# Performance work log

Measured on AMD Instinct MI355X. Metric: run time of the kernel, lower is better.

The kernel has to match this reference:

```python
import jax, jax.numpy as jnp
import numpy as np

NEG_SLOPE = 0.2
NEG_INF = -1e9


def _gat_branch(x, src, dst, edge_type, t, W, a_src, a_dst, b):
    """Single-head PyG GATConv restricted (by masking) to edges with edge_type == t,
    with self-loops added (PyG default add_self_loops=True)."""
    N = x.shape[0]
    h = x @ W                                   # [N, out_dim]
    s = h @ a_src                               # [N] source attention term
    d = h @ a_dst                               # [N] destination attention term
    # real edges (masked by type)
    e_edge = jax.nn.leaky_relu(s[src] + d[dst], NEG_SLOPE)
    e_edge = jnp.where(edge_type == t, e_edge, NEG_INF)
    # self-loop edges i -> i
    e_self = jax.nn.leaky_relu(s + d, NEG_SLOPE)
    dst_all = jnp.concatenate([dst, jnp.arange(N)])          # [E+N]
    e_all = jnp.concatenate([e_edge, e_self])                 # [E+N]
    # softmax over incoming edges per destination node (segment softmax)
    m = jax.ops.segment_max(e_all, dst_all, num_segments=N)
    p = jnp.exp(e_all - m[dst_all])
    denom = jax.ops.segment_sum(p, dst_all, num_segments=N)
    alpha = p / denom[dst_all]                                 # [E+N]
    msg = jnp.concatenate([h[src], h], axis=0) * alpha[:, None]
    return jax.ops.segment_sum(msg, dst_all, num_segments=N) + b


def setup_inputs() -> dict:
    key = jax.random.key(0)
    ks = jax.random.split(key, 12)
    N, E, in_dim, out_dim = 100000, 1000000, 64, 64
    glorot = (6.0 / (in_dim + out_dim)) ** 0.5
    att = (6.0 / (1 + out_dim)) ** 0.5
    return {
        "x": jax.random.normal(ks[0], (N, in_dim), dtype=jnp.float32),
        "edge_index": jax.random.randint(ks[1], (2, E), 0, N),
        "edge_type": jax.random.randint(ks[2], (E,), 0, 2),
        "W_login": jax.random.uniform(ks[3], (in_dim, out_dim), jnp.float32, -glorot, glorot),
        "a_src_login": jax.random.uniform(ks[4], (out_dim,), jnp.float32, -att, att),
        "a_dst_login": jax.random.uniform(ks[5], (out_dim,), jnp.float32, -att, att),
        "b_login": jnp.zeros((out_dim,), jnp.float32),
        "W_exec": jax.random.uniform(ks[6], (in_dim, out_dim), jnp.float32, -glorot, glorot),
        "a_src_exec": jax.random.uniform(ks[7], (out_dim,), jnp.float32, -att, att),
        "a_dst_exec": jax.random.uniform(ks[8], (out_dim,), jnp.float32, -att, att),
        "b_exec": jnp.zeros((out_dim,), jnp.float32),
    }


def reference(x, edge_index, edge_type, W_login, a_src_login, a_dst_login, b_login,
              W_exec, a_src_exec, a_dst_exec, b_exec):
    src, dst = edge_index[0], edge_index[1]
    out = _gat_branch(x, src, dst, edge_type, 0, W_login, a_src_login, a_dst_login, b_login)
    out = out + _gat_branch(x, src, dst, edge_type, 1, W_exec, a_src_exec, a_dst_exec, b_exec)
    return out
```

## Files before the change

### kernel.cpp

```cpp
#include <hip/hip_runtime.h>

#define D 64
#define CAP 896
#define BINB 64

typedef unsigned short u16;
typedef __attribute__((ext_vector_type(8))) __bf16 bf16x8;
typedef __attribute__((ext_vector_type(4))) float f32x4;

__device__ __forceinline__ float lrelu(float x) { return x > 0.f ? x : 0.2f * x; }
__device__ __forceinline__ u16 f2bf(float f) {
    unsigned u = __float_as_uint(f);
    return (u16)((u + 0x7fffu + ((u >> 16) & 1u)) >> 16);
}
__device__ __forceinline__ float bf2f(u16 v) { return __uint_as_float((unsigned)v << 16); }
__device__ __forceinline__ unsigned pack2(float lo, float hi) {
    return (unsigned)f2bf(lo) | ((unsigned)f2bf(hi) << 16);
}
__device__ __forceinline__ float blo(unsigned u) { return __uint_as_float(u << 16); }
__device__ __forceinline__ float bhi(unsigned u) { return __uint_as_float(u & 0xffff0000u); }

__global__ __launch_bounds__(256) void k_gemm3(
    const float* __restrict__ x,
    const float* __restrict__ W0, const float* __restrict__ as0, const float* __restrict__ ad0,
    const float* __restrict__ W1, const float* __restrict__ as1, const float* __restrict__ ad1,
    u16* __restrict__ hb, float* __restrict__ s_tab, float* __restrict__ d_tab,
    int* __restrict__ bktcnt, int nbk, int N, int ntiles)
{
    __shared__ u16 Wb[2][64][64];
    __shared__ u16 Xb[64][72];
    __shared__ float wsd[4][64];

    const int tid = threadIdx.x;
    if (blockIdx.x == 0)
        for (int i = tid; i < nbk; i += 256) bktcnt[i] = 0;

    for (int i = tid; i < 4096; i += 256) {
        const int k = i >> 6, n = i & 63;
        Wb[0][n][k] = f2bf(W0[i]);
        Wb[1][n][k] = f2bf(W1[i]);
    }
    {
        const int k = tid & 63;
        const int v = tid >> 6;
        const float* Ws = (v < 2) ? W0 : W1;
        const float* av = (v == 0) ? as0 : (v == 1) ? ad0 : (v == 2) ? as1 : ad1;
        float q = 0.f;
        for (int n = 0; n < 64; ++n) q = fmaf(Ws[(k << 6) + n], av[n], q);
        wsd[v][k] = q;
    }
    __syncthreads();

    const int lane = tid & 63;
    const int nl = lane & 15, quad = lane >> 4;
    const int wv = tid >> 6;

    bf16x8 bfrag[2][4][2];
#pragma unroll
    for (int br = 0; br < 2; ++br)
#pragma unroll
        for (int t = 0; t < 4; ++t)
#pragma unroll
            for (int h = 0; h < 2; ++h)
                bfrag[br][t][h] = *(const bf16x8*)&Wb[br][t * 16 + nl][h * 32 + quad * 8];

    const int rstage = tid >> 2;
    const int kc = (tid & 3) << 4;

    for (int tile = blockIdx.x; tile < ntiles; tile += gridDim.x) {
        const long n0 = (long)tile << 6;
        __syncthreads();
        {
            long row = n0 + rstage; if (row >= N) row = N - 1;
            const float4* xp = (const float4*)(x + row * D + kc);
            const float4 v0 = xp[0], v1 = xp[1], v2 = xp[2], v3 = xp[3];

            unsigned q[8];
            q[0] = pack2(v0.x, v0.y); q[1] = pack2(v0.z, v0.w);
            q[2] = pack2(v1.x, v1.y); q[3] = pack2(v1.z, v1.w);
            q[4] = pack2(v2.x, v2.y); q[5] = pack2(v2.z, v2.w);
            q[6] = pack2(v3.x, v3.y); q[7] = pack2(v3.z, v3.w);
            *(uint4*)&Xb[rstage][kc]     = make_uint4(q[0], q[1], q[2], q[3]);
            *(uint4*)&Xb[rstage][kc + 8] = make_uint4(q[4], q[5], q[6], q[7]);

            float ps[4];
#pragma unroll
            for (int v = 0; v < 4; ++v) {
                const float4* wp = (const float4*)&wsd[v][kc];
                const float4 wa = wp[0], wb = wp[1], wc = wp[2], wd = wp[3];
                float s = 0.f;
                s = fmaf(v0.x, wa.x, s); s = fmaf(v0.y, wa.y, s);
                s = fmaf(v0.z, wa.z, s); s = fmaf(v0.w, wa.w, s);
                s = fmaf(v1.x, wb.x, s); s = fmaf(v1.y, wb.y, s);
                s = fmaf(v1.z, wb.z, s); s = fmaf(v1.w, wb.w, s);
                s = fmaf(v2.x, wc.x, s); s = fmaf(v2.y, wc.y, s);
                s = fmaf(v2.z, wc.z, s); s = fmaf(v2.w, wc.w, s);
                s = fmaf(v3.x, wd.x, s); s = fmaf(v3.y, wd.y, s);
                s = fmaf(v3.z, wd.z, s); s = fmaf(v3.w, wd.w, s);
                ps[v] = s;
            }
#pragma unroll
            for (int v = 0; v < 4; ++v) {
                ps[v] += __shfl_xor(ps[v], 1, 64);
                ps[v] += __shfl_xor(ps[v], 2, 64);
            }
            const long rw = n0 + rstage;
            if ((tid & 3) == 0 && rw < N) {
                s_tab[(rw << 1)]     = ps[0]; d_tab[(rw << 1)]     = ps[1];
                s_tab[(rw << 1) | 1] = ps[2]; d_tab[(rw << 1) | 1] = ps[3];
            }
        }
        __syncthreads();

        const int rbase = wv << 4;
        const bf16x8 a0 = *(const bf16x8*)&Xb[rbase + nl][quad * 8];
        const bf16x8 a1 = *(const bf16x8*)&Xb[rbase + nl][32 + quad * 8];

        f32x4 acc[2][4];
#pragma unroll
        for (int br = 0; br < 2; ++br)
#pragma unroll
            for (int t = 0; t < 4; ++t) {
                f32x4 c = {0.f, 0.f, 0.f, 0.f};
                c = __builtin_amdgcn_mfma_f32_16x16x32_bf16(a0, bfrag[br][t][0], c, 0, 0, 0);
                c = __builtin_amdgcn_mfma_f32_16x16x32_bf16(a1, bfrag[br][t][1], c, 0, 0, 0);
                acc[br][t] = c;
            }

#pragma unroll
        for (int reg = 0; reg < 4; ++reg) {
            const long row = n0 + rbase + (quad << 2) + reg;
            if (row < N) {
#pragma unroll
                for (int br = 0; br < 2; ++br) {
                    u16* dp = hb + (((row << 1) | br) << 6) + nl;
                    dp[0]  = f2bf(acc[br][0][reg]);
                    dp[16] = f2bf(acc[br][1][reg]);
                    dp[32] = f2bf(acc[br][2][reg]);
                    dp[48] = f2bf(acc[br][3][reg]);
                }
            }
        }
    }
}

__global__ __launch_bounds__(256) void k_bin1(
    const int* __restrict__ src, const int* __restrict__ dst,
    const int* __restrict__ et, int* __restrict__ bktcnt,
    unsigned* __restrict__ bkt, int E, int nbk, int Eseg)
{
    extern __shared__ int cnt_l[];
    const int tid = threadIdx.x;
    for (int i = tid; i < nbk; i += 256) cnt_l[i] = 0;
    __syncthreads();

    const long e0 = (long)blockIdx.x * Eseg;
    const long e1 = min(e0 + (long)Eseg, (long)E);

    long i = e0 + tid;
    for (; i + 256 * 7 < e1; i += 256 * 8) {
        int d[8];
#pragma unroll
        for (int k = 0; k < 8; ++k) d[k] = dst[i + 256 * k];
#pragma unroll
        for (int k = 0; k < 8; ++k) atomicAdd(&cnt_l[d[k] >> 6], 1);
    }
    for (; i < e1; i += 256) atomicAdd(&cnt_l[dst[i] >> 6], 1);
    __syncthreads();

    for (int j = tid; j < nbk; j += 256) {
        const int c = cnt_l[j];
        cnt_l[j] = c ? atomicAdd(bktcnt + j, c) : 0;
    }
    __syncthreads();

    i = e0 + tid;
    for (; i + 256 * 7 < e1; i += 256 * 8) {
        int d[8];
#pragma unroll
        for (int k = 0; k < 8; ++k) d[k] = dst[i + 256 * k];
#pragma unroll
        for (int k = 0; k < 8; ++k) {
            const int bb = d[k] >> 6;
            const long ii = i + 256 * k;
            const int slot = atomicAdd(&cnt_l[bb], 1);
            if (slot < CAP)
                bkt[(long)bb * CAP + slot] =
                    ((unsigned)(d[k] & 63) << 18) | ((unsigned)src[ii] << 1) | (unsigned)et[ii];
        }
    }
    for (; i < e1; i += 256) {
        const int d = dst[i];
        const int bb = d >> 6;
        const int slot = atomicAdd(&cnt_l[bb], 1);
        if (slot < CAP)
            bkt[(long)bb * CAP + slot] =
                ((unsigned)(d & 63) << 18) | ((unsigned)src[i] << 1) | (unsigned)et[i];
    }
}

__global__ __launch_bounds__(256) void k_proc(
    const int* __restrict__ bktcnt, const unsigned* __restrict__ bkt,
    const float* __restrict__ s_tab, const float* __restrict__ d_tab,
    const u16* __restrict__ hb,
    const float* __restrict__ b0, const float* __restrict__ b1,
    float* __restrict__ out, int N)
{
    __shared__ unsigned tok[CAP];
    __shared__ int degl[64];
    __shared__ int curl[64];

    const int tid = threadIdx.x;
    const int b = blockIdx.x;
    const int lo = b << 6;
    const int cnt_nodes = min(64, N - lo);
    const int nb = min(bktcnt[b], CAP);

    if (tid < 64) degl[tid] = 0;
    __syncthreads();

    unsigned pr[4];
    int ns = 0;
    for (int i = tid; i < nb; i += 256) {
        const unsigned p = bkt[(long)b * CAP + i];
        pr[ns++] = p;
        atomicAdd(&degl[(p >> 18) & 63], 1);
    }
    __syncthreads();
    if (tid < 64) {
        int v = degl[tid];
        const int orig = v;
#pragma unroll
        for (int o = 1; o < 64; o <<= 1) {
            const int u = __shfl_up(v, o, 64);
            if (tid >= o) v += u;
        }
        curl[tid] = v - orig;
    }
    __syncthreads();
    for (int k = 0, i = tid; k < ns; i += 256, ++k) {
        const unsigned p = pr[k];
        const int s = atomicAdd(&curl[(p >> 18) & 63], 1);
        tok[s] = p & 0x3FFFFu;
    }
    __syncthreads();

    const int lane = tid & 63;
    const int wave = tid >> 6;
    const int q = lane >> 4;
    const int cl = lane & 15;

    for (int ni = wave; ni < cnt_nodes; ni += 4) {
        const int n = lo + ni;
        const int deg = degl[ni];
        const int off = curl[ni] - deg;
        const float d0n = d_tab[(n << 1)];
        const float d1n = d_tab[(n << 1) | 1];

        if (deg <= 62) {
            const int cnt = deg + 2;
            unsigned cmb = 0; unsigned t = 0; float e = 0.f;
            if (lane < deg) {
                cmb = tok[off + lane];
                t = cmb & 1u;
                e = lrelu(s_tab[cmb] + (t ? d1n : d0n));
            } else if (lane == deg)   { cmb = (unsigned)(n << 1);      t = 0; e = lrelu(s_tab[cmb] + d0n); }
            else if (lane == deg + 1) { cmb = (unsigned)(n << 1) | 1u; t = 1; e = lrelu(s_tab[cmb] + d1n); }

            const bool act = lane < cnt;
            const float p = act ? __expf(e) : 0.f;
            float p0 = t ? 0.f : p;
            float p1 = t ? p : 0.f;
#pragma unroll
            for (int o = 32; o; o >>= 1) {
                p0 += __shfl_xor(p0, o, 64);
                p1 += __shfl_xor(p1, o, 64);
            }
            const float a_r = act ? p / (t ? p1 : p0) : 0.f;

            float4 acc = {0.f, 0.f, 0.f, 0.f};
            const int nq = (cnt + 3) >> 2;
            int pp = 0;
            for (; pp + 1 < nq; pp += 2) {
                const int iA = (pp << 2) + q;
                const int iB = iA + 4;
                const int iBc = iB < cnt ? iB : cnt - 1;
                float aA    = __shfl(a_r, iA, 64);
                unsigned cA = __shfl(cmb, iA, 64);
                float aB    = __shfl(a_r, iBc, 64);
                unsigned cB = __shfl(cmb, iBc, 64);
                if (iB >= cnt) aB = 0.f;
                const uint2 uA = *(const uint2*)(hb + ((long)cA << 6) + (cl << 2));
                const uint2 uB = *(const uint2*)(hb + ((long)cB << 6) + (cl << 2));
                acc.x = fmaf(aA, blo(uA.x), acc.x);
                acc.y = fmaf(aA, bhi(uA.x), acc.y);
                acc.z = fmaf(aA, blo(uA.y), acc.z);
                acc.w = fmaf(aA, bhi(uA.y), acc.w);
                acc.x = fmaf(aB, blo(uB.x), acc.x);
                acc.y = fmaf(aB, bhi(uB.x), acc.y);
                acc.z = fmaf(aB, blo(uB.y), acc.z);
                acc.w = fmaf(aB, bhi(uB.y), acc.w);
            }
            if (pp < nq) {
                const int iA = (pp << 2) + q;
                const int iAc = iA < cnt ? iA : cnt - 1;
                float aA    = __shfl(a_r, iAc, 64);
                unsigned cA = __shfl(cmb, iAc, 64);
                if (iA >= cnt) aA = 0.f;
                const uint2 uA = *(const uint2*)(hb + ((long)cA << 6) + (cl << 2));
                acc.x = fmaf(aA, blo(uA.x), acc.x);
                acc.y = fmaf(aA, bhi(uA.x), acc.y);
                acc.z = fmaf(aA, blo(uA.y), acc.z);
                acc.w = fmaf(aA, bhi(uA.y), acc.w);
            }
            acc.x += __shfl_xor(acc.x, 16, 64);
            acc.y += __shfl_xor(acc.y, 16, 64);
            acc.z += __shfl_xor(acc.z, 16, 64);
            acc.w += __shfl_xor(acc.w, 16, 64);
            acc.x += __shfl_xor(acc.x, 32, 64);
            acc.y += __shfl_xor(acc.y, 32, 64);
            acc.z += __shfl_xor(acc.z, 32, 64);
            acc.w += __shfl_xor(acc.w, 32, 64);
            if (lane < 16) {
                const int c0 = cl << 2;
                float4 o;
                o.x = acc.x + b0[c0]     + b1[c0];
                o.y = acc.y + b0[c0 + 1] + b1[c0 + 1];
                o.z = acc.z + b0[c0 + 2] + b1[c0 + 2];
                o.w = acc.w + b0[c0 + 3] + b1[c0 + 3];
                *(float4*)(out + ((long)n << 6) + c0) = o;
            }
        } else {
            const float es0 = lrelu(s_tab[(n << 1)] + d0n);
            const float es1 = lrelu(s_tab[(n << 1) | 1] + d1n);
            float p0 = 0.f, p1 = 0.f;
            for (int j = lane; j < deg; j += 64) {
                const unsigned c = tok[off + j];
                const float e = lrelu(s_tab[c] + ((c & 1u) ? d1n : d0n));
                if (c & 1u) p1 += __expf(e); else p0 += __expf(e);
            }
#pragma unroll
            for (int o = 32; o; o >>= 1) {
                p0 += __shfl_xor(p0, o, 64);
                p1 += __shfl_xor(p1, o, 64);
            }
            const float den0 = p0 + __expf(es0);
            const float den1 = p1 + __expf(es1);

            float acc = (__expf(es0) / den0) * bf2f(hb[((long)n << 7) + lane])
                      + (__expf(es1) / den1) * bf2f(hb[((long)n << 7) + 64 + lane]);
            for (int base = 0; base < deg; base += 64) {
                const int j = base + lane;
                unsigned ck = 0; float a = 0.f;
                if (j < deg) {
                    ck = tok[off + j];
                    const float e = lrelu(s_tab[ck] + ((ck & 1u) ? d1n : d0n));
                    a = __expf(e) / ((ck & 1u) ? den1 : den0);
                }
                const int lim = min(64, deg - base);
                for (int jj = 0; jj < lim; ++jj) {
                    const float aj = __shfl(a, jj, 64);
                    const unsigned cj = __shfl(ck, jj, 64);
                    acc = fmaf(aj, bf2f(hb[((long)cj << 6) + lane]), acc);
                }
            }
            out[((long)n << 6) + lane] = acc + b0[lane] + b1[lane];
        }
    }
}

extern "C" void kernel_launch(void* const* d_in, const int* in_sizes, int n_in,
                              void* d_out, int out_size, void* d_ws, size_t ws_size,
                              hipStream_t stream) {
    const float* x   = (const float*)d_in[0];
    const int*   ei  = (const int*)d_in[1];
    const int*   et  = (const int*)d_in[2];
    const float* W0  = (const float*)d_in[3];
    const float* as0 = (const float*)d_in[4];
    const float* ad0 = (const float*)d_in[5];
    const float* b0  = (const float*)d_in[6];
    const float* W1  = (const float*)d_in[7];
    const float* as1 = (const float*)d_in[8];
    const float* ad1 = (const float*)d_in[9];
    const float* b1  = (const float*)d_in[10];
    float* out = (float*)d_out;

    const int N = in_sizes[0] / D;
    const int E = in_sizes[1] / 2;
    const int* src = ei;
    const int* dst = ei + E;

    const int nbk = (N + 63) >> 6;

    char* w = (char*)d_ws;
    u16* hb = (u16*)w;            w += (size_t)2 * N * D * sizeof(u16);
    float* s_tab = (float*)w;     w += (size_t)2 * N * sizeof(float);
    float* d_tab = (float*)w;     w += (size_t)2 * N * sizeof(float);
    int* bktcnt = (int*)w;        w += (size_t)nbk * sizeof(int);
    unsigned* bkt = (unsigned*)w; w += (size_t)nbk * CAP * sizeof(unsigned);

    const int ntiles = (N + 63) / 64;
    const int Eseg = (E + BINB - 1) / BINB;

    k_gemm3<<<768, 256, 0, stream>>>(x, W0, as0, ad0, W1, as1, ad1,
                                     hb, s_tab, d_tab, bktcnt, nbk, N, ntiles);
    k_bin1<<<BINB, 256, (size_t)nbk * sizeof(int), stream>>>(
        src, dst, et, bktcnt, bkt, E, nbk, Eseg);
    k_proc<<<nbk, 256, 0, stream>>>(bktcnt, bkt, s_tab, d_tab, hb, b0, b1, out, N);
}
```

Before: 205.0 us.

## Fuse GEMM and edge binning into one concurrent launch; widen aggregation blocks

The edge-binning kernel now runs as 64 extra blocks inside the GEMM launch, so binning overlaps with the projection GEMM instead of running after it. The binning blocks reuse the GEMM's weight shared-memory buffer as their per-bucket counters. Bucket counters are now zeroed with a memset on the stream, because the fused launch can no longer clear them itself. The aggregation kernel moves to 512 threads per block (8 waves per bucket) to add parallelism, at the cost of an extra memset launch and heavier per-block resource use.

Measured after the change: 212.7 us. 1.04x slower.

```diff
diff --git a/kernel.cpp b/kernel.cpp
--- a/kernel.cpp
+++ b/kernel.cpp
@@ -2,7 +2,8 @@
 
 #define D 64
 #define CAP 896
-#define BINB 64
+#define GEMM_BLKS 768
+#define BIN_BLKS 64
 
 typedef unsigned short u16;
 typedef __attribute__((ext_vector_type(8))) __bf16 bf16x8;
@@ -20,20 +21,72 @@
 __device__ __forceinline__ float blo(unsigned u) { return __uint_as_float(u << 16); }
 __device__ __forceinline__ float bhi(unsigned u) { return __uint_as_float(u & 0xffff0000u); }
 
-__global__ __launch_bounds__(256) void k_gemm3(
+__global__ __launch_bounds__(256) void k_fused(
     const float* __restrict__ x,
     const float* __restrict__ W0, const float* __restrict__ as0, const float* __restrict__ ad0,
     const float* __restrict__ W1, const float* __restrict__ as1, const float* __restrict__ ad1,
     u16* __restrict__ hb, float* __restrict__ s_tab, float* __restrict__ d_tab,
-    int* __restrict__ bktcnt, int nbk, int N, int ntiles)
+    const int* __restrict__ src, const int* __restrict__ dst, const int* __restrict__ et,
+    int* __restrict__ bktcnt, unsigned* __restrict__ bkt,
+    int E, int nbk, int Eseg, int N, int ntiles)
 {
     __shared__ u16 Wb[2][64][64];
     __shared__ u16 Xb[64][72];
     __shared__ float wsd[4][64];
 
     const int tid = threadIdx.x;
-    if (blockIdx.x == 0)
-        for (int i = tid; i < nbk; i += 256) bktcnt[i] = 0;
+
+    if (blockIdx.x >= GEMM_BLKS) {
+        int* cnt_l = (int*)&Wb[0][0][0];
+        for (int i = tid; i < nbk; i += 256) cnt_l[i] = 0;
+        __syncthreads();
+
+        const int bb_ = blockIdx.x - GEMM_BLKS;
+        const long e0 = (long)bb_ * Eseg;
+        const long e1 = min(e0 + (long)Eseg, (long)E);
+
+        long i = e0 + tid;
+        for (; i + 256 * 7 < e1; i += 256 * 8) {
+            int d[8];
+#pragma unroll
+            for (int k = 0; k < 8; ++k) d[k] = dst[i + 256 * k];
+#pragma unroll
+            for (int k = 0; k < 8; ++k) atomicAdd(&cnt_l[d[k] >> 6], 1);
+        }
+        for (; i < e1; i += 256) atomicAdd(&cnt_l[dst[i] >> 6], 1);
+        __syncthreads();
+
+        for (int j = tid; j < nbk; j += 256) {
+            const int c = cnt_l[j];
+            cnt_l[j] = c ? atomicAdd(bktcnt + j, c) : 0;
+        }
+        __syncthreads();
+
+        i = e0 + tid;
+        for (; i + 256 * 7 < e1; i += 256 * 8) {
+            int d[8];
+#pragma unroll
+            for (int k = 0; k < 8; ++k) d[k] = dst[i + 256 * k];
+#pragma unroll
+            for (int k = 0; k < 8; ++k) {
+                const int bb = d[k] >> 6;
+                const long ii = i + 256 * k;
+                const int slot = atomicAdd(&cnt_l[bb], 1);
+                if (slot < CAP)
+                    bkt[(long)bb * CAP + slot] =
+                        ((unsigned)(d[k] & 63) << 18) | ((unsigned)src[ii] << 1) | (unsigned)et[ii];
+            }
+        }
+        for (; i < e1; i += 256) {
+            const int d = dst[i];
+            const int bb = d >> 6;
+            const int slot = atomicAdd(&cnt_l[bb], 1);
+            if (slot < CAP)
+                bkt[(long)bb * CAP + slot] =
+                    ((unsigned)(d & 63) << 18) | ((unsigned)src[i] << 1) | (unsigned)et[i];
+        }
+        return;
+    }
 
     for (int i = tid; i < 4096; i += 256) {
         const int k = i >> 6, n = i & 63;
@@ -67,7 +120,7 @@
     const int rstage = tid >> 2;
     const int kc = (tid & 3) << 4;
 
-    for (int tile = blockIdx.x; tile < ntiles; tile += gridDim.x) {
+    for (int tile = blockIdx.x; tile < ntiles; tile += GEMM_BLKS) {
         const long n0 = (long)tile << 6;
         __syncthreads();
         {
@@ -144,62 +197,7 @@
     }
 }
 
-__global__ __launch_bounds__(256) void k_bin1(
-    const int* __restrict__ src, const int* __restrict__ dst,
-    const int* __restrict__ et, int* __restrict__ bktcnt,
-    unsigned* __restrict__ bkt, int E, int nbk, int Eseg)
-{
-    extern __shared__ int cnt_l[];
-    const int tid = threadIdx.x;
-    for (int i = tid; i < nbk; i += 256) cnt_l[i] = 0;
-    __syncthreads();
-
-    const long e0 = (long)blockIdx.x * Eseg;
-    const long e1 = min(e0 + (long)Eseg, (long)E);
-
-    long i = e0 + tid;
-    for (; i + 256 * 7 < e1; i += 256 * 8) {
-        int d[8];
-#pragma unroll
-        for (int k = 0; k < 8; ++k) d[k] = dst[i + 256 * k];
-#pragma unroll
-        for (int k = 0; k < 8; ++k) atomicAdd(&cnt_l[d[k] >> 6], 1);
-    }
-    for (; i < e1; i += 256) atomicAdd(&cnt_l[dst[i] >> 6], 1);
-    __syncthreads();
-
-    for (int j = tid; j < nbk; j += 256) {
-        const int c = cnt_l[j];
-        cnt_l[j] = c ? atomicAdd(bktcnt + j, c) : 0;
-    }
-    __syncthreads();
-
-    i = e0 + tid;
-    for (; i + 256 * 7 < e1; i += 256 * 8) {
-        int d[8];
-#pragma unroll
-        for (int k = 0; k < 8; ++k) d[k] = dst[i + 256 * k];
-#pragma unroll
-        for (int k = 0; k < 8; ++k) {
-            const int bb = d[k] >> 6;
-            const long ii = i + 256 * k;
-            const int slot = atomicAdd(&cnt_l[bb], 1);
-            if (slot < CAP)
-                bkt[(long)bb * CAP + slot] =
-                    ((unsigned)(d[k] & 63) << 18) | ((unsigned)src[ii] << 1) | (unsigned)et[ii];
-        }
-    }
-    for (; i < e1; i += 256) {
-        const int d = dst[i];
-        const int bb = d >> 6;
-        const int slot = atomicAdd(&cnt_l[bb], 1);
-        if (slot < CAP)
-            bkt[(long)bb * CAP + slot] =
-                ((unsigned)(d & 63) << 18) | ((unsigned)src[i] << 1) | (unsigned)et[i];
-    }
-}
-
-__global__ __launch_bounds__(256) void k_proc(
+__global__ __launch_bounds__(512) void k_proc(
     const int* __restrict__ bktcnt, const unsigned* __restrict__ bkt,
     const float* __restrict__ s_tab, const float* __restrict__ d_tab,
     const u16* __restrict__ hb,
@@ -219,9 +217,9 @@
     if (tid < 64) degl[tid] = 0;
     __syncthreads();
 
-    unsigned pr[4];
+    unsigned pr[2];
     int ns = 0;
-    for (int i = tid; i < nb; i += 256) {
+    for (int i = tid; i < nb; i += 512) {
         const unsigned p = bkt[(long)b * CAP + i];
         pr[ns++] = p;
         atomicAdd(&degl[(p >> 18) & 63], 1);
@@ -238,7 +236,7 @@
         curl[tid] = v - orig;
     }
     __syncthreads();
-    for (int k = 0, i = tid; k < ns; i += 256, ++k) {
+    for (int k = 0, i = tid; k < ns; i += 512, ++k) {
         const unsigned p = pr[k];
         const int s = atomicAdd(&curl[(p >> 18) & 63], 1);
         tok[s] = p & 0x3FFFFu;
@@ -250,7 +248,7 @@
     const int q = lane >> 4;
     const int cl = lane & 15;
 
-    for (int ni = wave; ni < cnt_nodes; ni += 4) {
+    for (int ni = wave; ni < cnt_nodes; ni += 8) {
         const int n = lo + ni;
         const int deg = degl[ni];
         const int off = curl[ni] - deg;
@@ -400,11 +398,11 @@
     unsigned* bkt = (unsigned*)w; w += (size_t)nbk * CAP * sizeof(unsigned);
 
     const int ntiles = (N + 63) / 64;
-    const int Eseg = (E + BINB - 1) / BINB;
-
-    k_gemm3<<<768, 256, 0, stream>>>(x, W0, as0, ad0, W1, as1, ad1,
-                                     hb, s_tab, d_tab, bktcnt, nbk, N, ntiles);
-    k_bin1<<<BINB, 256, (size_t)nbk * sizeof(int), stream>>>(
-        src, dst, et, bktcnt, bkt, E, nbk, Eseg);
-    k_proc<<<nbk, 256, 0, stream>>>(bktcnt, bkt, s_tab, d_tab, hb, b0, b1, out, N);
+    const int Eseg = (E + BIN_BLKS - 1) / BIN_BLKS;
+
+    hipMemsetAsync(bktcnt, 0, (size_t)nbk * sizeof(int), stream);
+    k_fused<<<GEMM_BLKS + BIN_BLKS, 256, 0, stream>>>(
+        x, W0, as0, ad0, W1, as1, ad1, hb, s_tab, d_tab,
+        src, dst, et, bktcnt, bkt, E, nbk, Eseg, N, ntiles);
+    k_proc<<<nbk, 512, 0, stream>>>(bktcnt, bkt, s_tab, d_tab, hb, b0, b1, out, N);
 }
```

## Widen binning grid, vectorize h stores with permuted layout, enlarge proc blocks

Applied to the files above, without the earlier changes.

Raises the edge-binning grid from 64 to 256 blocks so more compute units share the scatter work. The GEMM now writes each row's bf16 outputs as one 8-byte packed store, using a column-interleaved layout; the aggregation kernel remaps its output columns to match. The aggregation kernel moves to 512-thread blocks (8 waves per 64-node bucket) and keeps the summed bias in shared memory. Bucket counters are now cleared with a memset instead of inside the GEMM. The costs are more blocks contending on the global bucket atomics and scalar rather than float4 output stores in the fast path.

After: 195.0 us. 4.9% less time.

```diff
diff --git a/kernel.cpp b/kernel.cpp
--- a/kernel.cpp
+++ b/kernel.cpp
@@ -2,7 +2,7 @@
 
 #define D 64
 #define CAP 896
-#define BINB 64
+#define BINB 256
 
 typedef unsigned short u16;
 typedef __attribute__((ext_vector_type(8))) __bf16 bf16x8;
@@ -25,15 +25,13 @@
     const float* __restrict__ W0, const float* __restrict__ as0, const float* __restrict__ ad0,
     const float* __restrict__ W1, const float* __restrict__ as1, const float* __restrict__ ad1,
     u16* __restrict__ hb, float* __restrict__ s_tab, float* __restrict__ d_tab,
-    int* __restrict__ bktcnt, int nbk, int N, int ntiles)
+    int N, int ntiles)
 {
     __shared__ u16 Wb[2][64][64];
     __shared__ u16 Xb[64][72];
     __shared__ float wsd[4][64];
 
     const int tid = threadIdx.x;
-    if (blockIdx.x == 0)
-        for (int i = tid; i < nbk; i += 256) bktcnt[i] = 0;
 
     for (int i = tid; i < 4096; i += 256) {
         const int k = i >> 6, n = i & 63;
@@ -133,11 +131,10 @@
             if (row < N) {
 #pragma unroll
                 for (int br = 0; br < 2; ++br) {
-                    u16* dp = hb + (((row << 1) | br) << 6) + nl;
-                    dp[0]  = f2bf(acc[br][0][reg]);
-                    dp[16] = f2bf(acc[br][1][reg]);
-                    dp[32] = f2bf(acc[br][2][reg]);
-                    dp[48] = f2bf(acc[br][3][reg]);
+                    uint2 v;
+                    v.x = pack2(acc[br][0][reg], acc[br][1][reg]);
+                    v.y = pack2(acc[br][2][reg], acc[br][3][reg]);
+                    *(uint2*)(hb + (((row << 1) | br) << 6) + (nl << 2)) = v;
                 }
             }
         }
@@ -199,7 +196,7 @@
     }
 }
 
-__global__ __launch_bounds__(256) void k_proc(
+__global__ __launch_bounds__(512) void k_proc(
     const int* __restrict__ bktcnt, const unsigned* __restrict__ bkt,
     const float* __restrict__ s_tab, const float* __restrict__ d_tab,
     const u16* __restrict__ hb,
@@ -209,6 +206,7 @@
     __shared__ unsigned tok[CAP];
     __shared__ int degl[64];
     __shared__ int curl[64];
+    __shared__ float bsum[64];
 
     const int tid = threadIdx.x;
     const int b = blockIdx.x;
@@ -216,12 +214,12 @@
     const int cnt_nodes = min(64, N - lo);
     const int nb = min(bktcnt[b], CAP);
 
-    if (tid < 64) degl[tid] = 0;
-    __syncthreads();
-
-    unsigned pr[4];
+    if (tid < 64) { degl[tid] = 0; bsum[tid] = b0[tid] + b1[tid]; }
+    __syncthreads();
+
+    unsigned pr[2];
     int ns = 0;
-    for (int i = tid; i < nb; i += 256) {
+    for (int i = tid; i < nb; i += 512) {
         const unsigned p = bkt[(long)b * CAP + i];
         pr[ns++] = p;
         atomicAdd(&degl[(p >> 18) & 63], 1);
@@ -238,7 +236,7 @@
         curl[tid] = v - orig;
     }
     __syncthreads();
-    for (int k = 0, i = tid; k < ns; i += 256, ++k) {
+    for (int k = 0, i = tid; k < ns; i += 512, ++k) {
         const unsigned p = pr[k];
         const int s = atomicAdd(&curl[(p >> 18) & 63], 1);
         tok[s] = p & 0x3FFFFu;
@@ -250,7 +248,7 @@
     const int q = lane >> 4;
     const int cl = lane & 15;
 
-    for (int ni = wave; ni < cnt_nodes; ni += 4) {
+    for (int ni = wave; ni < cnt_nodes; ni += 8) {
         const int n = lo + ni;
         const int deg = degl[ni];
         const int off = curl[ni] - deg;
@@ -322,15 +320,14 @@
             acc.z += __shfl_xor(acc.z, 32, 64);
             acc.w += __shfl_xor(acc.w, 32, 64);
             if (lane < 16) {
-                const int c0 = cl << 2;
-                float4 o;
-                o.x = acc.x + b0[c0]     + b1[c0];
-                o.y = acc.y + b0[c0 + 1] + b1[c0 + 1];
-                o.z = acc.z + b0[c0 + 2] + b1[c0 + 2];
-                o.w = acc.w + b0[c0 + 3] + b1[c0 + 3];
-                *(float4*)(out + ((long)n << 6) + c0) = o;
+                float* op = out + ((long)n << 6);
+                op[cl]      = acc.x + bsum[cl];
+                op[16 + cl] = acc.y + bsum[16 + cl];
+                op[32 + cl] = acc.z + bsum[32 + cl];
+                op[48 + cl] = acc.w + bsum[48 + cl];
             }
         } else {
+            const int oc = ((lane & 3) << 4) + (lane >> 2);
             const float es0 = lrelu(s_tab[(n << 1)] + d0n);
             const float es1 = lrelu(s_tab[(n << 1) | 1] + d1n);
             float p0 = 0.f, p1 = 0.f;
@@ -364,7 +361,7 @@
                     acc = fmaf(aj, bf2f(hb[((long)cj << 6) + lane]), acc);
                 }
             }
-            out[((long)n << 6) + lane] = acc + b0[lane] + b1[lane];
+            out[((long)n << 6) + oc] = acc + bsum[oc];
         }
     }
 }
@@ -402,9 +399,10 @@
     const int ntiles = (N + 63) / 64;
     const int Eseg = (E + BINB - 1) / BINB;
 
+    hipMemsetAsync(bktcnt, 0, (size_t)nbk * sizeof(int), stream);
     k_gemm3<<<768, 256, 0, stream>>>(x, W0, as0, ad0, W1, as1, ad1,
-                                     hb, s_tab, d_tab, bktcnt, nbk, N, ntiles);
+                                     hb, s_tab, d_tab, N, ntiles);
     k_bin1<<<BINB, 256, (size_t)nbk * sizeof(int), stream>>>(
         src, dst, et, bktcnt, bkt, E, nbk, Eseg);
-    k_proc<<<nbk, 256, 0, stream>>>(bktcnt, bkt, s_tab, d_tab, hb, b0, b1, out, N);
-}
+    k_proc<<<nbk, 512, 0, stream>>>(bktcnt, bkt, s_tab, d_tab, hb, b0, b1, out, N);
+}
```
